# Optimization experiments

Measured on AMD Instinct MI355X. Metric: run time of the kernel, lower is better.

## Reference

```python
import jax, jax.numpy as jnp
import numpy as np

B, L, V, E_ENC, D_DEC, E_EMB = 256, 128, 4096, 1024, 1024, 512


def _lin(key, out_f, in_f, scale=0.02):
    k1, k2 = jax.random.split(key)
    return (jax.random.normal(k1, (out_f, in_f), jnp.float32) * scale,
            jax.random.normal(k2, (out_f,), jnp.float32) * scale)


def setup_inputs() -> dict:
    key = jax.random.key(0)
    ks = jax.random.split(key, 12)
    x = jax.random.normal(ks[0], (B, 1, V), jnp.float32)
    hidden = jax.random.normal(ks[1], (1, B, D_DEC), jnp.float32)
    enc_output = jax.random.normal(ks[2], (B, L, E_ENC), jnp.float32)
    W1_w, W1_b = _lin(ks[3], D_DEC, E_ENC)
    W2_w, W2_b = _lin(ks[4], D_DEC, D_DEC)
    V_w, V_b = _lin(ks[5], 1, D_DEC)
    out2emb_w, out2emb_b = _lin(ks[6], E_EMB, V)
    gru_wi, gru_bi = _lin(ks[7], 3 * D_DEC, E_EMB + E_ENC)
    gru_wh, gru_bh = _lin(ks[8], 3 * D_DEC, D_DEC)
    fc1_w, fc1_b = _lin(ks[9], E_EMB, D_DEC)
    fc2_w, fc2_b = _lin(ks[10], V, E_EMB)
    return dict(x=x, hidden=hidden, enc_output=enc_output,
                W1_w=W1_w, W1_b=W1_b, W2_w=W2_w, W2_b=W2_b, V_w=V_w, V_b=V_b,
                out2emb_w=out2emb_w, out2emb_b=out2emb_b,
                gru_wi=gru_wi, gru_wh=gru_wh, gru_bi=gru_bi, gru_bh=gru_bh,
                fc1_w=fc1_w, fc1_b=fc1_b, fc2_w=fc2_w, fc2_b=fc2_b)


def reference(x, hidden, enc_output, W1_w, W1_b, W2_w, W2_b, V_w, V_b,
              out2emb_w, out2emb_b, gru_wi, gru_wh, gru_bi, gru_bh,
              fc1_w, fc1_b, fc2_w, fc2_b):
    # --- Bahdanau additive attention ---
    h_t = hidden[-1][:, None, :]                                   # (B,1,dec)
    score = jnp.tanh(enc_output @ W1_w.T + W1_b + h_t @ W2_w.T + W2_b)  # (B,L,dec)
    attn = jax.nn.softmax(score @ V_w.T + V_b, axis=1)             # (B,L,1)
    context = jnp.sum(attn * enc_output, axis=1)                   # (B,enc)
    # --- embed previous output distribution ---
    x_emb = x @ out2emb_w.T + out2emb_b                            # (B,1,emb)
    rnn_in = jnp.concatenate([context[:, None, :], x_emb], -1)[:, 0, :]  # (B,emb+enc)
    # --- single GRU step (PyTorch gate layout r,z,n) ---
    h0 = hidden[0]
    gi = rnn_in @ gru_wi.T + gru_bi
    gh = h0 @ gru_wh.T + gru_bh
    ir, iz, inn = jnp.split(gi, 3, axis=-1)
    hr, hz, hn = jnp.split(gh, 3, axis=-1)
    r = jax.nn.sigmoid(ir + hr)
    z = jax.nn.sigmoid(iz + hz)
    n = jnp.tanh(inn + r * hn)
    h_new = (1.0 - z) * n + z * h0                                 # (B,dec)
    # --- output MLP ---
    out = jnp.tanh(h_new @ fc1_w.T + fc1_b) @ fc2_w.T + fc2_b      # (B,vocab)
    return out, h_new[None], attn
```

## Files before the change

kernel.cpp:

```cpp
#include <hip/hip_runtime.h>
#include <math.h>


#define B_   256
#define L_   128
#define V_   4096
#define ENC_ 1024
#define DEC_ 1024
#define EMB_ 512
#define MB_  1048576ull

typedef __bf16 bf16;
typedef __bf16 bf16x8 __attribute__((ext_vector_type(8)));
typedef __bf16 bf16x4 __attribute__((ext_vector_type(4)));
typedef float  f32x4  __attribute__((ext_vector_type(4)));

__device__ __forceinline__ float fast_tanh(float x) {
  float e = __builtin_amdgcn_exp2f(x * 2.88539008177792681472f);
  return 1.0f - 2.0f * __builtin_amdgcn_rcpf(e + 1.0f);
}
__device__ __forceinline__ float fast_sigmoid(float x) {
  return __builtin_amdgcn_rcpf(1.0f + __builtin_amdgcn_exp2f(-1.44269504088896f * x));
}

__device__ __forceinline__ void cp16(const void* g, void* l) {
  __builtin_amdgcn_global_load_lds(
      (const __attribute__((address_space(1))) void*)g,
      (__attribute__((address_space(3))) void*)l,
      16, 0, 0);
}

__device__ __forceinline__ bf16x8 ld8f(const float* f) {
  f32x4 a = *(const f32x4*)f;
  f32x4 b = *(const f32x4*)(f + 4);
  bf16x8 r;
  r[0] = (bf16)a[0]; r[1] = (bf16)a[1]; r[2] = (bf16)a[2]; r[3] = (bf16)a[3];
  r[4] = (bf16)b[0]; r[5] = (bf16)b[1]; r[6] = (bf16)b[2]; r[7] = (bf16)b[3];
  return r;
}


__device__ __forceinline__ void gemm64_f32(
    const float* __restrict__ A, const float* __restrict__ Brow,
    int strideA, int strideB, int kbeg, int kend, int row0,
    bf16* As, bf16* Bs, f32x4 acc[4])
{
  const int t   = threadIdx.x;
  const int lane = t & 63, w = t >> 6, q = lane >> 4, c16 = lane & 15;
  const int sr  = t >> 3, lb = t & 7;

  for (int k0 = kbeg; k0 < kend; k0 += 64) {
    bf16x8 va[2], vb[2];
#pragma unroll
    for (int ch = 0; ch < 2; ch++) {
      int r    = ch * 32 + sr;
      int gcol = k0 + ((lb ^ (r & 7)) << 3);
      va[ch] = ld8f(A    + (size_t)(row0 + r) * strideA + gcol);
      vb[ch] = ld8f(Brow + (size_t)r * strideB + gcol);
    }
#pragma unroll
    for (int ch = 0; ch < 2; ch++) {
      *(bf16x8*)&As[ch * 2048 + t * 8] = va[ch];
      *(bf16x8*)&Bs[ch * 2048 + t * 8] = vb[ch];
    }
    __syncthreads();
#pragma unroll
    for (int kkb = 0; kkb < 8; kkb += 4) {
      int rb = w * 16 + c16;
      bf16x8 bfr = *(const bf16x8*)&Bs[rb * 64 + (((kkb + q) ^ (rb & 7)) << 3)];
#pragma unroll
      for (int i = 0; i < 4; i++) {
        int ra = i * 16 + c16;
        bf16x8 af = *(const bf16x8*)&As[ra * 64 + (((kkb + q) ^ (ra & 7)) << 3)];
        acc[i] = __builtin_amdgcn_mfma_f32_16x16x32_bf16(af, bfr, acc[i], 0, 0, 0);
      }
    }
    __syncthreads();
  }
}

__global__ __launch_bounds__(256) void setup_k(
    const float* __restrict__ hidden, const float* __restrict__ W2,
    const float* __restrict__ wh, const float* __restrict__ W1_b,
    const float* __restrict__ W2_b, const float* __restrict__ gbh,
    const float* __restrict__ x, const float* __restrict__ o2e,
    const float* __restrict__ enc, const float* __restrict__ W1,
    const float* __restrict__ wi, const float* __restrict__ fc1w,
    const float* __restrict__ fc2w,
    bf16* __restrict__ enc_bf, bf16* __restrict__ W1_bf,
    bf16* __restrict__ wi_bf, bf16* __restrict__ fc1_bf,
    bf16* __restrict__ fc2_bf,
    bf16* __restrict__ u, bf16* __restrict__ gh, float* __restrict__ xe4)
{
  __shared__ __align__(16) bf16 As[64 * 64];
  __shared__ __align__(16) bf16 Bs[64 * 64];

  const int bid = blockIdx.x;
  const int t   = threadIdx.x;

  if (bid >= 384) {
    int i = bid - 384;
    const float* src; bf16* dst; int blk;
    if      (i < 8192) { src = enc;  dst = enc_bf; blk = i; }
    else if (i < 8448) { src = W1;   dst = W1_bf;  blk = i - 8192; }
    else if (i < 9600) { src = wi;   dst = wi_bf;  blk = i - 8448; }
    else if (i < 9728) { src = fc1w; dst = fc1_bf; blk = i - 9600; }
    else               { src = fc2w; dst = fc2_bf; blk = i - 9728; }
    const size_t base = (size_t)blk * 4096 + t * 16;
    const float* s = src + base;
    bf16* d = dst + base;
    *(bf16x8*)(d)     = ld8f(s);
    *(bf16x8*)(d + 8) = ld8f(s + 8);
    return;
  }

  const int lane = t & 63, w = t >> 6, q = lane >> 4, c16 = lane & 15;
  f32x4 acc[4] = {};

  if (bid < 256) {
    const int row0 = (bid >> 6) * 64;
    const int col0 = (bid & 63) * 64;
    const bool isU = (col0 < 1024);
    const float* Brow = isU ? (W2 + (size_t)col0 * 1024)
                            : (wh + (size_t)(col0 - 1024) * 1024);
    gemm64_f32(hidden, Brow, 1024, 1024, 0, 1024, row0, As, Bs, acc);

    const int gc = col0 + w * 16 + c16;
    float bias = isU ? (W1_b[gc] + W2_b[gc]) : gbh[gc - 1024];
#pragma unroll
    for (int i = 0; i < 4; i++) {
      int gr0 = row0 + i * 16 + q * 4;
#pragma unroll
      for (int r = 0; r < 4; r++) {
        float v = acc[i][r] + bias;
        if (isU) u[(size_t)(gr0 + r) * 1024 + gc] = (bf16)v;
        else     gh[(size_t)(gr0 + r) * 3072 + (gc - 1024)] = (bf16)v;
      }
    }
  } else {
    const int i3   = bid - 256;
    const int col0 = (i3 & 7) * 64;
    const int row0 = ((i3 >> 3) & 3) * 64;
    const int z    = i3 >> 5;
    gemm64_f32(x, o2e + (size_t)col0 * 4096, 4096, 4096,
               z * 1024, z * 1024 + 1024, row0, As, Bs, acc);

    const int gc = col0 + w * 16 + c16;
    float* out = xe4 + (size_t)z * 131072;
#pragma unroll
    for (int i = 0; i < 4; i++) {
      int gr0 = row0 + i * 16 + q * 4;
#pragma unroll
      for (int r = 0; r < 4; r++)
        out[(size_t)(gr0 + r) * 512 + gc] = acc[i][r];
    }
  }
}

__device__ __forceinline__ void stage_half(
    const bf16* __restrict__ src, bf16* dst, int grow0, int k0, int t)
{
  const int sr = t >> 3, lb = t & 7;
#pragma unroll
  for (int ch = 0; ch < 2; ch++) {
    int r    = ch * 64 + sr;
    int gcol = k0 + ((lb ^ (r & 7)) << 3);
    cp16(src + (size_t)(grow0 + r) * 1024 + gcol, dst + r * 64 + lb * 8);
  }
}

#define BAR()   __builtin_amdgcn_s_barrier()
#define SB0()   __builtin_amdgcn_sched_barrier(0)
#define LGKM8() { asm volatile("s_waitcnt lgkmcnt(8)" ::: "memory"); SB0(); }
#define LGKM4() { asm volatile("s_waitcnt lgkmcnt(4)" ::: "memory"); SB0(); }
#define LGKM0() { asm volatile("s_waitcnt lgkmcnt(0)" ::: "memory"); SB0(); }
#define VM2()   asm volatile("s_waitcnt vmcnt(2)" ::: "memory")
#define VM4()   asm volatile("s_waitcnt vmcnt(4)" ::: "memory")

#define RD_A4(dst, base, ib, kq)                                            \
  _Pragma("unroll") for (int i = 0; i < 4; i++) {                           \
    const int ra = ra_base + ((ib) + i) * 16;                               \
    dst[i] = *(const bf16x8*)&(base)[ra * 64 + (((kq) ^ (ra & 7)) << 3)];   \
  }
#define RD_B4(dst, base, kq)                                                \
  _Pragma("unroll") for (int j = 0; j < 4; j++) {                           \
    const int rb = rb_base + j * 16;                                        \
    dst[j] = *(const bf16x8*)&(base)[rb * 64 + (((kq) ^ (rb & 7)) << 3)];   \
  }
#define MFMA16(ib, afv, bv)                                                 \
  __builtin_amdgcn_s_setprio(1);                                            \
  _Pragma("unroll") for (int i = 0; i < 4; i++)                             \
    _Pragma("unroll") for (int j = 0; j < 4; j++)                           \
      acc[(ib) + i][j] = __builtin_amdgcn_mfma_f32_16x16x32_bf16(           \
          afv[i], bv[j], acc[(ib) + i][j], 0, 0, 0);                        \
  __builtin_amdgcn_s_setprio(0);

__global__ __launch_bounds__(512, 2) void score_8p(
    const bf16* __restrict__ A,
    const bf16* __restrict__ Bw,
    const bf16* __restrict__ u,
    const float* __restrict__ Vw,
    float* __restrict__ e_part)
{
  __shared__ __align__(16) bf16 sA0[16384];
  __shared__ __align__(16) bf16 sA1[16384];
  __shared__ __align__(16) bf16 sB0[16384];
  __shared__ __align__(16) bf16 sB1[16384];
  __shared__ float s_part[4][256];

  const int t = threadIdx.x;
  const int wg  = blockIdx.x;
  const int swz = (wg & 7) * 64 + (wg >> 3);
  const int bx  = swz & 3;
  const int by  = swz >> 2;
  const int row0 = by * 256;
  const int col0 = bx * 256;

  const int lane = t & 63, w = t >> 6;
  const int wm = w >> 2, wn = w & 3;
  const int q = lane >> 4, c16 = lane & 15;
  const int rb_base = wn * 64 + c16;
  const int ra_base = wm * 128 + c16;

  bf16x8 afA[4], afB[4], b0[4], b1[4];
  f32x4 acc[8][4] = {};

  stage_half(A,  sA0,        row0,       0,  t);
  stage_half(A,  sA0 + 8192, row0 + 128, 0,  t);
  stage_half(Bw, sB0,        col0,       0,  t);
  stage_half(Bw, sB0 + 8192, col0 + 128, 0,  t);
  stage_half(Bw, sB1,        col0,       64, t);
  stage_half(Bw, sB1 + 8192, col0 + 128, 64, t);
  VM4();
  BAR(); SB0();
  RD_A4(afA, sA0, 0, q);
  RD_B4(b0, sB0, q);

  for (int k = 0; k < 8; ++k) {
    const int e = 2 * k, o = 2 * k + 1;
    const bool nl = (k < 7);

    RD_A4(afB, sA0, 0, 4 + q);
    RD_B4(b1, sB0, 4 + q);
    stage_half(A, sA1, row0, o * 64, t);
    LGKM8();
    MFMA16(0, afA, b0);
    BAR();

    RD_A4(afA, sA0, 4, q);
    stage_half(A, sA1 + 8192, row0 + 128, o * 64, t);
    LGKM4();
    MFMA16(0, afB, b1);
    BAR();

    RD_A4(afB, sA0, 4, 4 + q);
    if (nl) stage_half(Bw, sB0, col0, (e + 2) * 64, t);
    LGKM4();
    MFMA16(4, afA, b0);
    VM2();
    BAR();

    RD_A4(afA, sA1, 0, q);
    RD_B4(b0, sB1, q);
    if (nl) stage_half(Bw, sB0 + 8192, col0 + 128, (e + 2) * 64, t);
    LGKM8();
    MFMA16(4, afB, b1);
    BAR();

    RD_A4(afB, sA1, 0, 4 + q);
    RD_B4(b1, sB1, 4 + q);
    if (nl) stage_half(A, sA0, row0, (e + 2) * 64, t);
    LGKM8();
    MFMA16(0, afA, b0);
    BAR();

    RD_A4(afA, sA1, 4, q);
    if (nl) stage_half(A, sA0 + 8192, row0 + 128, (e + 2) * 64, t);
    LGKM4();
    MFMA16(0, afB, b1);
    BAR();

    RD_A4(afB, sA1, 4, 4 + q);
    if (nl) stage_half(Bw, sB1, col0, (o + 2) * 64, t);
    LGKM4();
    MFMA16(4, afA, b0);
    VM2();
    BAR();

    if (nl) {
      RD_A4(afA, sA0, 0, q);
      RD_B4(b0, sB0, q);
      stage_half(Bw, sB1 + 8192, col0 + 128, (o + 2) * 64, t);
      LGKM8();
    } else {
      LGKM0();
    }
    MFMA16(4, afB, b1);
    BAR();
  }

  const int b = by * 2 + wm;
  float uc[4], vw[4];
#pragma unroll
  for (int j = 0; j < 4; j++) {
    const int gc = col0 + wn * 64 + j * 16 + c16;
    uc[j] = (float)u[b * 1024 + gc];
    vw[j] = Vw[gc];
  }
  float rsum[8][4];
#pragma unroll
  for (int i = 0; i < 8; i++) {
#pragma unroll
    for (int r = 0; r < 4; r++) {
      float v = 0.0f;
#pragma unroll
      for (int j = 0; j < 4; j++)
        v += fast_tanh(acc[i][j][r] + uc[j]) * vw[j];
      v += __shfl_xor(v, 1);
      v += __shfl_xor(v, 2);
      v += __shfl_xor(v, 4);
      v += __shfl_xor(v, 8);
      rsum[i][r] = v;
    }
  }
#pragma unroll
  for (int i = 0; i < 8; i++)
#pragma unroll
    for (int r = 0; r < 4; r++)
      if (c16 == 0) s_part[wn][wm * 128 + i * 16 + q * 4 + r] = rsum[i][r];
  __syncthreads();
  if (t < 256)
    e_part[(size_t)bx * 32768 + row0 + t] =
        s_part[0][t] + s_part[1][t] + s_part[2][t] + s_part[3][t];
}

__global__ __launch_bounds__(256) void softmax_f(
    const float* __restrict__ e_part,
    const bf16* __restrict__ enc,
    const float* __restrict__ xe4,
    const float* __restrict__ o2eb,
    float* __restrict__ attn_out,
    bf16* __restrict__ rnn_in)
{
  const int b = blockIdx.x;
  const int t = threadIdx.x;
  __shared__ float se[128];

  if (t < 128) {
    float s = 0.0f;
#pragma unroll
    for (int cb = 0; cb < 4; cb++) s += e_part[(size_t)cb * 32768 + b * 128 + t];
    se[t] = s;
  }
  __syncthreads();

  float m = -1e30f;
  for (int l = 0; l < 128; l++) m = fmaxf(m, se[l]);
  float sum = 0.0f;
  for (int l = 0; l < 128; l++) sum += expf(se[l] - m);
  float inv = 1.0f / sum;
  __syncthreads();
  if (t < 128) {
    float p = expf(se[t] - m) * inv;
    attn_out[b * 128 + t] = p;
    se[t] = p;
  }
  __syncthreads();

  float a0 = 0, a1 = 0, a2 = 0, a3 = 0;
  const bf16* ep = enc + (size_t)b * L_ * ENC_ + t * 4;
  for (int l = 0; l < 128; l++) {
    float p = se[l];
    bf16x4 v = *(const bf16x4*)(ep + (size_t)l * ENC_);
    a0 += p * (float)v[0]; a1 += p * (float)v[1];
    a2 += p * (float)v[2]; a3 += p * (float)v[3];
  }
  bf16x4 o;
  o[0] = (bf16)a0; o[1] = (bf16)a1; o[2] = (bf16)a2; o[3] = (bf16)a3;
  *(bf16x4*)(rnn_in + (size_t)b * 1536 + t * 4) = o;

#pragma unroll
  for (int jj = 0; jj < 2; jj++) {
    int j = jj * 256 + t;
    float v = o2eb[j];
#pragma unroll
    for (int z = 0; z < 4; z++) v += xe4[(size_t)z * 131072 + b * 512 + j];
    rnn_in[(size_t)b * 1536 + 1024 + j] = (bf16)v;
  }
}

template <int ACT, int OUTF32>
__global__ __launch_bounds__(256) void gemm_f(
    const bf16* __restrict__ A, const bf16* __restrict__ Bw,
    const float* __restrict__ bias1,
    void* __restrict__ C, int K, int out_ld)
{
  __shared__ __align__(16) bf16 As[64 * 64];
  __shared__ __align__(16) bf16 Bs[64 * 64];

  const int t    = threadIdx.x;
  const int lane = t & 63;
  const int w    = t >> 6;
  const int q    = lane >> 4;
  const int c16  = lane & 15;
  const int sr   = t >> 3;
  const int lb   = t & 7;
  const int row0 = blockIdx.y * 64;
  const int col0 = blockIdx.x * 64;

  f32x4 acc[4] = {};

  for (int k0 = 0; k0 < K; k0 += 64) {
#pragma unroll
    for (int ch = 0; ch < 2; ch++) {
      int r    = ch * 32 + sr;
      int gcol = k0 + ((lb ^ (r & 7)) << 3);
      cp16(A  + (size_t)(row0 + r) * K + gcol, &As[ch * 2048 + t * 8]);
      cp16(Bw + (size_t)(col0 + r) * K + gcol, &Bs[ch * 2048 + t * 8]);
    }
    __syncthreads();
#pragma unroll
    for (int kkb = 0; kkb < 8; kkb += 4) {
      int rb = w * 16 + c16;
      bf16x8 bfr = *(const bf16x8*)&Bs[rb * 64 + (((kkb + q) ^ (rb & 7)) << 3)];
#pragma unroll
      for (int i = 0; i < 4; i++) {
        int ra = i * 16 + c16;
        bf16x8 af = *(const bf16x8*)&As[ra * 64 + (((kkb + q) ^ (ra & 7)) << 3)];
        acc[i] = __builtin_amdgcn_mfma_f32_16x16x32_bf16(af, bfr, acc[i], 0, 0, 0);
      }
    }
    __syncthreads();
  }

  const int gc = col0 + w * 16 + c16;
  float bias = bias1[gc];
#pragma unroll
  for (int i = 0; i < 4; i++) {
    int gr0 = row0 + i * 16 + q * 4;
#pragma unroll
    for (int r = 0; r < 4; r++) {
      float v = acc[i][r] + bias;
      if (ACT == 1) v = fast_tanh(v);
      size_t off = (size_t)(gr0 + r) * out_ld + gc;
      if (OUTF32) ((float*)C)[off] = v;
      else        ((bf16*)C)[off] = (bf16)v;
    }
  }
}

__global__ __launch_bounds__(256) void gru_f(
    const bf16* __restrict__ gi, const bf16* __restrict__ gh,
    const float* __restrict__ h0,
    float* __restrict__ hnew_out, bf16* __restrict__ hnew_i)
{
  int idx = blockIdx.x * 256 + threadIdx.x;
  int b = idx >> 10, d = idx & 1023;
  const bf16* gib = gi + b * 3072;
  const bf16* ghb = gh + b * 3072;
  float ir = (float)gib[d], iz = (float)gib[1024 + d], in = (float)gib[2048 + d];
  float hr = (float)ghb[d], hz = (float)ghb[1024 + d], hn = (float)ghb[2048 + d];
  float r = fast_sigmoid(ir + hr);
  float z = fast_sigmoid(iz + hz);
  float n = fast_tanh(in + r * hn);
  float h = (1.0f - z) * n + z * h0[idx];
  hnew_out[idx] = h;
  hnew_i[idx]   = (bf16)h;
}

extern "C" void kernel_launch(void* const* d_in, const int* in_sizes, int n_in,
                              void* d_out, int out_size, void* d_ws, size_t ws_size,
                              hipStream_t stream) {
  const float* x      = (const float*)d_in[0];
  const float* hidden = (const float*)d_in[1];
  const float* enc    = (const float*)d_in[2];
  const float* W1_w   = (const float*)d_in[3];
  const float* W1_b   = (const float*)d_in[4];
  const float* W2_w   = (const float*)d_in[5];
  const float* W2_b   = (const float*)d_in[6];
  const float* V_w    = (const float*)d_in[7];
  const float* o2e_w  = (const float*)d_in[9];
  const float* o2e_b  = (const float*)d_in[10];
  const float* gru_wi = (const float*)d_in[11];
  const float* gru_wh = (const float*)d_in[12];
  const float* gru_bi = (const float*)d_in[13];
  const float* gru_bh = (const float*)d_in[14];
  const float* fc1_w  = (const float*)d_in[15];
  const float* fc1_b  = (const float*)d_in[16];
  const float* fc2_w  = (const float*)d_in[17];
  const float* fc2_b  = (const float*)d_in[18];

  float* out_main = (float*)d_out;
  float* out_h    = out_main + (size_t)B_ * V_;
  float* out_attn = out_h + (size_t)B_ * DEC_;

  char* ws = (char*)d_ws;
  bf16*  enc_bf  = (bf16*)(ws);
  bf16*  W1_bf   = (bf16*)(ws + 64 * MB_);
  bf16*  wi_bf   = (bf16*)(ws + 66 * MB_);
  bf16*  fc1_bf  = (bf16*)(ws + 75 * MB_);
  bf16*  fc2_bf  = (bf16*)(ws + 76 * MB_);
  bf16*  u_bf    = (bf16*)(ws + 80 * MB_);
  bf16*  gh_bf   = (bf16*)(ws + 80 * MB_ + 524288);
  float* e_part  = (float*)(ws + 82 * MB_);
  bf16*  gi_bf   = (bf16*)(ws + 82 * MB_ + 524288);
  bf16*  rnn_in  = (bf16*)(ws + 84 * MB_);
  bf16*  tbuf    = (bf16*)(ws + 84 * MB_ + 786432);
  bf16*  hnew_bf = (bf16*)(ws + 85 * MB_);
  float* xe4     = (float*)(ws + 85 * MB_ + 524288);

  setup_k<<<10624, 256, 0, stream>>>(
      hidden, W2_w, gru_wh, W1_b, W2_b, gru_bh, x, o2e_w,
      enc, W1_w, gru_wi, fc1_w, fc2_w,
      enc_bf, W1_bf, wi_bf, fc1_bf, fc2_bf, u_bf, gh_bf, xe4);

  score_8p<<<512, 512, 0, stream>>>(enc_bf, W1_bf, u_bf, V_w, e_part);

  softmax_f<<<B_, 256, 0, stream>>>(e_part, enc_bf, xe4, o2e_b, out_attn, rnn_in);

  gemm_f<0, 0><<<dim3(48, 4), 256, 0, stream>>>(rnn_in, wi_bf, gru_bi, gi_bf, 1536, 3072);

  gru_f<<<(B_ * DEC_) / 256, 256, 0, stream>>>(gi_bf, gh_bf, hidden, out_h, hnew_bf);

  gemm_f<1, 0><<<dim3(8, 4), 256, 0, stream>>>(hnew_bf, fc1_bf, fc1_b, tbuf, 1024, 512);

  gemm_f<0, 1><<<dim3(64, 4), 256, 0, stream>>>(tbuf, fc2_bf, fc2_b, out_main, 512, 4096);
}
```

Baseline: 412.6 us.

## Prefetch setup GEMM tiles, grid-stride conversion, relax score waits, split context accumulators

```diff
diff --git a/kernel.cpp b/kernel.cpp
--- a/kernel.cpp
+++ b/kernel.cpp
@@ -40,7 +40,7 @@
 }
 
 
-__device__ __forceinline__ void gemm64_f32(
+__device__ __forceinline__ void gemm64_pipe(
     const float* __restrict__ A, const float* __restrict__ Brow,
     int strideA, int strideB, int kbeg, int kend, int row0,
     bf16* As, bf16* Bs, f32x4 acc[4])
@@ -49,21 +49,31 @@
   const int lane = t & 63, w = t >> 6, q = lane >> 4, c16 = lane & 15;
   const int sr  = t >> 3, lb = t & 7;
 
+  bf16x8 va[2], vb[2];
+#pragma unroll
+  for (int ch = 0; ch < 2; ch++) {
+    int r    = ch * 32 + sr;
+    int gcol = kbeg + ((lb ^ (r & 7)) << 3);
+    va[ch] = ld8f(A    + (size_t)(row0 + r) * strideA + gcol);
+    vb[ch] = ld8f(Brow + (size_t)r * strideB + gcol);
+  }
+
   for (int k0 = kbeg; k0 < kend; k0 += 64) {
-    bf16x8 va[2], vb[2];
-#pragma unroll
-    for (int ch = 0; ch < 2; ch++) {
-      int r    = ch * 32 + sr;
-      int gcol = k0 + ((lb ^ (r & 7)) << 3);
-      va[ch] = ld8f(A    + (size_t)(row0 + r) * strideA + gcol);
-      vb[ch] = ld8f(Brow + (size_t)r * strideB + gcol);
-    }
 #pragma unroll
     for (int ch = 0; ch < 2; ch++) {
       *(bf16x8*)&As[ch * 2048 + t * 8] = va[ch];
       *(bf16x8*)&Bs[ch * 2048 + t * 8] = vb[ch];
     }
     __syncthreads();
+    if (k0 + 64 < kend) {
+#pragma unroll
+      for (int ch = 0; ch < 2; ch++) {
+        int r    = ch * 32 + sr;
+        int gcol = k0 + 64 + ((lb ^ (r & 7)) << 3);
+        va[ch] = ld8f(A    + (size_t)(row0 + r) * strideA + gcol);
+        vb[ch] = ld8f(Brow + (size_t)r * strideB + gcol);
+      }
+    }
 #pragma unroll
     for (int kkb = 0; kkb < 8; kkb += 4) {
       int rb = w * 16 + c16;
@@ -99,18 +109,19 @@
   const int t   = threadIdx.x;
 
   if (bid >= 384) {
-    int i = bid - 384;
-    const float* src; bf16* dst; int blk;
-    if      (i < 8192) { src = enc;  dst = enc_bf; blk = i; }
-    else if (i < 8448) { src = W1;   dst = W1_bf;  blk = i - 8192; }
-    else if (i < 9600) { src = wi;   dst = wi_bf;  blk = i - 8448; }
-    else if (i < 9728) { src = fc1w; dst = fc1_bf; blk = i - 9600; }
-    else               { src = fc2w; dst = fc2_bf; blk = i - 9728; }
-    const size_t base = (size_t)blk * 4096 + t * 16;
-    const float* s = src + base;
-    bf16* d = dst + base;
-    *(bf16x8*)(d)     = ld8f(s);
-    *(bf16x8*)(d + 8) = ld8f(s + 8);
+    for (int c = bid - 384; c < 10240; c += 1664) {
+      const float* src; bf16* dst; int blk;
+      if      (c < 8192) { src = enc;  dst = enc_bf; blk = c; }
+      else if (c < 8448) { src = W1;   dst = W1_bf;  blk = c - 8192; }
+      else if (c < 9600) { src = wi;   dst = wi_bf;  blk = c - 8448; }
+      else if (c < 9728) { src = fc1w; dst = fc1_bf; blk = c - 9600; }
+      else               { src = fc2w; dst = fc2_bf; blk = c - 9728; }
+      const size_t base = (size_t)blk * 4096 + t * 16;
+      const float* s = src + base;
+      bf16* d = dst + base;
+      *(bf16x8*)(d)     = ld8f(s);
+      *(bf16x8*)(d + 8) = ld8f(s + 8);
+    }
     return;
   }
 
@@ -123,7 +134,7 @@
     const bool isU = (col0 < 1024);
     const float* Brow = isU ? (W2 + (size_t)col0 * 1024)
                             : (wh + (size_t)(col0 - 1024) * 1024);
-    gemm64_f32(hidden, Brow, 1024, 1024, 0, 1024, row0, As, Bs, acc);
+    gemm64_pipe(hidden, Brow, 1024, 1024, 0, 1024, row0, As, Bs, acc);
 
     const int gc = col0 + w * 16 + c16;
     float bias = isU ? (W1_b[gc] + W2_b[gc]) : gbh[gc - 1024];
@@ -142,8 +153,8 @@
     const int col0 = (i3 & 7) * 64;
     const int row0 = ((i3 >> 3) & 3) * 64;
     const int z    = i3 >> 5;
-    gemm64_f32(x, o2e + (size_t)col0 * 4096, 4096, 4096,
-               z * 1024, z * 1024 + 1024, row0, As, Bs, acc);
+    gemm64_pipe(x, o2e + (size_t)col0 * 4096, 4096, 4096,
+                z * 1024, z * 1024 + 1024, row0, As, Bs, acc);
 
     const int gc = col0 + w * 16 + c16;
     float* out = xe4 + (size_t)z * 131072;
@@ -170,12 +181,10 @@
 }
 
 #define BAR()   __builtin_amdgcn_s_barrier()
-#define SB0()   __builtin_amdgcn_sched_barrier(0)
-#define LGKM8() { asm volatile("s_waitcnt lgkmcnt(8)" ::: "memory"); SB0(); }
-#define LGKM4() { asm volatile("s_waitcnt lgkmcnt(4)" ::: "memory"); SB0(); }
-#define LGKM0() { asm volatile("s_waitcnt lgkmcnt(0)" ::: "memory"); SB0(); }
+#define FENCE() asm volatile("" ::: "memory")
 #define VM2()   asm volatile("s_waitcnt vmcnt(2)" ::: "memory")
 #define VM4()   asm volatile("s_waitcnt vmcnt(4)" ::: "memory")
+#define PHASE_END() { FENCE(); BAR(); FENCE(); }
 
 #define RD_A4(dst, base, ib, kq)                                            \
   _Pragma("unroll") for (int i = 0; i < 4; i++) {                           \
@@ -232,7 +241,7 @@
   stage_half(Bw, sB1,        col0,       64, t);
   stage_half(Bw, sB1 + 8192, col0 + 128, 64, t);
   VM4();
-  BAR(); SB0();
+  PHASE_END();
   RD_A4(afA, sA0, 0, q);
   RD_B4(b0, sB0, q);
 
@@ -243,60 +252,50 @@
     RD_A4(afB, sA0, 0, 4 + q);
     RD_B4(b1, sB0, 4 + q);
     stage_half(A, sA1, row0, o * 64, t);
-    LGKM8();
     MFMA16(0, afA, b0);
-    BAR();
+    PHASE_END();
 
     RD_A4(afA, sA0, 4, q);
     stage_half(A, sA1 + 8192, row0 + 128, o * 64, t);
-    LGKM4();
     MFMA16(0, afB, b1);
-    BAR();
+    PHASE_END();
 
     RD_A4(afB, sA0, 4, 4 + q);
     if (nl) stage_half(Bw, sB0, col0, (e + 2) * 64, t);
-    LGKM4();
     MFMA16(4, afA, b0);
     VM2();
-    BAR();
+    PHASE_END();
 
     RD_A4(afA, sA1, 0, q);
     RD_B4(b0, sB1, q);
     if (nl) stage_half(Bw, sB0 + 8192, col0 + 128, (e + 2) * 64, t);
-    LGKM8();
     MFMA16(4, afB, b1);
-    BAR();
+    PHASE_END();
 
     RD_A4(afB, sA1, 0, 4 + q);
     RD_B4(b1, sB1, 4 + q);
     if (nl) stage_half(A, sA0, row0, (e + 2) * 64, t);
-    LGKM8();
     MFMA16(0, afA, b0);
-    BAR();
+    PHASE_END();
 
     RD_A4(afA, sA1, 4, q);
     if (nl) stage_half(A, sA0 + 8192, row0 + 128, (e + 2) * 64, t);
-    LGKM4();
     MFMA16(0, afB, b1);
-    BAR();
+    PHASE_END();
 
     RD_A4(afB, sA1, 4, 4 + q);
     if (nl) stage_half(Bw, sB1, col0, (o + 2) * 64, t);
-    LGKM4();
     MFMA16(4, afA, b0);
     VM2();
-    BAR();
+    PHASE_END();
 
     if (nl) {
       RD_A4(afA, sA0, 0, q);
       RD_B4(b0, sB0, q);
       stage_half(Bw, sB1 + 8192, col0 + 128, (o + 2) * 64, t);
-      LGKM8();
-    } else {
-      LGKM0();
     }
     MFMA16(4, afB, b1);
-    BAR();
+    PHASE_END();
   }
 
   const int b = by * 2 + wm;
@@ -367,16 +366,23 @@
   }
   __syncthreads();
 
-  float a0 = 0, a1 = 0, a2 = 0, a3 = 0;
+  float a0[4] = {}, a1[4] = {}, a2[4] = {}, a3[4] = {};
   const bf16* ep = enc + (size_t)b * L_ * ENC_ + t * 4;
-  for (int l = 0; l < 128; l++) {
-    float p = se[l];
-    bf16x4 v = *(const bf16x4*)(ep + (size_t)l * ENC_);
-    a0 += p * (float)v[0]; a1 += p * (float)v[1];
-    a2 += p * (float)v[2]; a3 += p * (float)v[3];
+#pragma unroll 1
+  for (int l = 0; l < 32; l++) {
+#pragma unroll
+    for (int s = 0; s < 4; s++) {
+      float p = se[l + s * 32];
+      bf16x4 v = *(const bf16x4*)(ep + (size_t)(l + s * 32) * ENC_);
+      a0[s] += p * (float)v[0]; a1[s] += p * (float)v[1];
+      a2[s] += p * (float)v[2]; a3[s] += p * (float)v[3];
+    }
   }
   bf16x4 o;
-  o[0] = (bf16)a0; o[1] = (bf16)a1; o[2] = (bf16)a2; o[3] = (bf16)a3;
+  o[0] = (bf16)(a0[0] + a0[1] + a0[2] + a0[3]);
+  o[1] = (bf16)(a1[0] + a1[1] + a1[2] + a1[3]);
+  o[2] = (bf16)(a2[0] + a2[1] + a2[2] + a2[3]);
+  o[3] = (bf16)(a3[0] + a3[1] + a3[2] + a3[3]);
   *(bf16x4*)(rnn_in + (size_t)b * 1536 + t * 4) = o;
 
 #pragma unroll
@@ -509,7 +515,7 @@
   bf16*  hnew_bf = (bf16*)(ws + 85 * MB_);
   float* xe4     = (float*)(ws + 85 * MB_ + 524288);
 
-  setup_k<<<10624, 256, 0, stream>>>(
+  setup_k<<<2048, 256, 0, stream>>>(
       hidden, W2_w, gru_wh, W1_b, W2_b, gru_bh, x, o2e_w,
       enc, W1_w, gru_wi, fc1_w, fc2_w,
       enc_bf, W1_bf, wi_bf, fc1_bf, fc2_bf, u_bf, gh_bf, xe4);
```

Result: slower. 424.1 us (+2.8%).
